# Performance work log

Hardware: AMD Instinct MI355X
Metric: run time of the kernel (lower is better)

Reference implementation:

```python
import jax, jax.numpy as jnp
import numpy as np

NEG = -1000000000.0
TEMP = 0.5
K = 15
EPS = 1e-5


def _bn(x, g, b):
    # BatchNorm1d in training mode: batch mean, biased variance
    mu = jnp.mean(x, axis=0)
    var = jnp.mean((x - mu) ** 2, axis=0)
    return (x - mu) * jax.lax.rsqrt(var + EPS) * g + b


def _lrelu(x):
    return jnp.where(x > 0, x, 0.2 * x)


def setup_inputs() -> dict:
    key = jax.random.key(0)
    ks = jax.random.split(key, 8)
    B, L = 131072, 50
    inp = {
        "z": jax.random.normal(ks[0], (B, L), jnp.float32),
        "u": jax.random.uniform(ks[1], (K, B, 25), jnp.float32),
        "W1": jax.random.normal(ks[2], (L, 128), jnp.float32) * 0.1,
        "b1": jnp.zeros((128,), jnp.float32),
        "g1": jnp.ones((128,), jnp.float32),
        "be1": jnp.zeros((128,), jnp.float32),
        "W2": jax.random.normal(ks[3], (128, 256), jnp.float32) * 0.1,
        "b2": jnp.zeros((256,), jnp.float32),
        "g2": jnp.ones((256,), jnp.float32),
        "be2": jnp.zeros((256,), jnp.float32),
        "W3": jax.random.normal(ks[4], (256, 128), jnp.float32) * 0.1,
        "b3": jnp.zeros((128,), jnp.float32),
        "g3": jnp.ones((128,), jnp.float32),
        "be3": jnp.zeros((128,), jnp.float32),
        "W4": jax.random.normal(ks[5], (128, 25), jnp.float32) * 0.1,
        "b4": jnp.zeros((25,), jnp.float32),
    }
    return inp


def reference(z, u, W1, b1, g1, be1, W2, b2, g2, be2, W3, b3, g3, be3, W4, b4):
    h = _lrelu(_bn(z @ W1 + b1, g1, be1))
    h = _lrelu(_bn(h @ W2 + b2, g2, be2))
    h = _lrelu(_bn(h @ W3 + b3, g3, be3))
    logits = h @ W4 + b4  # [B, 25]

    def step(mask, u_i):
        masked = jnp.where(mask, logits, NEG)
        noise = -jnp.log(-jnp.log(u_i))
        gumbel = (masked + noise) / TEMP
        probs = jax.nn.softmax(gumbel, axis=-1)
        idx = jnp.argmax(probs, axis=-1)  # [B]
        onehot = jax.nn.one_hot(idx, 25, dtype=bool)
        return mask & ~onehot, idx

    mask0 = jnp.ones(logits.shape, dtype=bool)
    _, idxs = jax.lax.scan(step, mask0, u)  # idxs: [K, B]
    selected = idxs.T.astype(jnp.float32) + 1.0  # [B, K], selected_idx + 1
    return (selected - 1.0) / 24.0
```

## Files before the change

kernel.cpp:

```cpp
#include <hip/hip_runtime.h>
#include <math.h>

#define BATCH 131072

template<int MT, int NT, int NSTORE, int TM, int TN, int BLK, bool AFFINE, bool STATS>
__global__ __launch_bounds__(BLK, 2)
void gemm_bn(const float* __restrict__ Ain, int K,
             const float* __restrict__ W, const float* __restrict__ bias,
             const float* __restrict__ sc, const float* __restrict__ sh,
             float* __restrict__ Xout,
             double* __restrict__ gsum, double* __restrict__ gsq)
{
    constexpr int KS  = 32;
    constexpr int MP  = MT + 4;
    constexpr int NP  = NT + 4;
    constexpr int NCG = NT / TN;
    constexpr int RG  = MT / TM;
    constexpr int NH  = TN / 4;
    static_assert(BLK == NCG * RG, "thread mapping");
    static_assert(!STATS || 2 * RG * NP <= KS * NP, "stats reuse of Bs");

    __shared__ float As[KS][MP];
    __shared__ float Bs[KS][NP];

    const int tid = threadIdx.x;
    const int r0  = blockIdx.x * MT;
    const int tx  = tid % NCG;
    const int ty  = tid / NCG;

    float acc[TM][TN] = {};

    const int KC = (K + KS - 1) / KS;
    for (int kc = 0; kc < KC; ++kc) {
        const int kbase = kc * KS;
        __syncthreads();
        constexpr int AL = MT * KS / BLK;
        #pragma unroll
        for (int l = 0; l < AL; ++l) {
            int idx = tid + l * BLK;
            int i = idx >> 5;
            int j = idx & 31;
            int gk = kbase + j;
            float v;
            if (AFFINE) {
                v = Ain[(size_t)(r0 + i) * K + gk];
                v = v * sc[gk] + sh[gk];
                v = v > 0.f ? v : 0.2f * v;
            } else {
                v = (gk < K) ? Ain[(size_t)(r0 + i) * K + gk] : 0.f;
            }
            As[j][i] = v;
        }
        constexpr int BL = NT * KS / BLK;
        #pragma unroll
        for (int l = 0; l < BL; ++l) {
            int idx = tid + l * BLK;
            int kk = idx / NT;
            int n  = idx % NT;
            int gk = kbase + kk;
            float v = 0.f;
            if (gk < K && n < NSTORE) v = W[(size_t)gk * NSTORE + n];
            Bs[kk][n] = v;
        }
        __syncthreads();
        #pragma unroll 2
        for (int k = 0; k < KS; ++k) {
            float a[TM], b[TN];
            #pragma unroll
            for (int i4 = 0; i4 < TM; i4 += 4)
                *reinterpret_cast<float4*>(&a[i4]) =
                    *reinterpret_cast<const float4*>(&As[k][ty * TM + i4]);
            #pragma unroll
            for (int h = 0; h < NH; ++h)
                *reinterpret_cast<float4*>(&b[h * 4]) =
                    *reinterpret_cast<const float4*>(&Bs[k][h * (NCG * 4) + tx * 4]);
            #pragma unroll
            for (int i = 0; i < TM; ++i)
                #pragma unroll
                for (int j = 0; j < TN; ++j)
                    acc[i][j] = fmaf(a[i], b[j], acc[i][j]);
        }
    }

    float bc[TN];
    #pragma unroll
    for (int j = 0; j < TN; ++j) {
        int gc = (j >> 2) * (NCG * 4) + tx * 4 + (j & 3);
        bc[j] = (gc < NSTORE) ? bias[gc] : 0.f;
    }
    float psum[TN] = {};
    float psq[TN]  = {};
    #pragma unroll
    for (int i = 0; i < TM; ++i) {
        int row = r0 + ty * TM + i;
        float x[TN];
        #pragma unroll
        for (int j = 0; j < TN; ++j) {
            x[j] = acc[i][j] + bc[j];
            psum[j] += x[j];
            psq[j]  += x[j] * x[j];
        }
        if (NSTORE == NT) {
            #pragma unroll
            for (int h = 0; h < NH; ++h) {
                float4 v = make_float4(x[h*4], x[h*4+1], x[h*4+2], x[h*4+3]);
                *reinterpret_cast<float4*>(
                    &Xout[(size_t)row * NSTORE + h * (NCG * 4) + tx * 4]) = v;
            }
        } else {
            #pragma unroll
            for (int j = 0; j < TN; ++j) {
                int gc = (j >> 2) * (NCG * 4) + tx * 4 + (j & 3);
                if (gc < NSTORE) Xout[(size_t)row * NSTORE + gc] = x[j];
            }
        }
    }

    if (STATS) {
        __syncthreads();
        float* S1 = &Bs[0][0];
        float* S2 = S1 + RG * NP;
        #pragma unroll
        for (int j = 0; j < TN; ++j) {
            int gc = (j >> 2) * (NCG * 4) + tx * 4 + (j & 3);
            S1[ty * NP + gc] = psum[j];
            S2[ty * NP + gc] = psq[j];
        }
        __syncthreads();
        if (tid < NT) {
            double s = 0.0, q = 0.0;
            #pragma unroll 4
            for (int t = 0; t < RG; ++t) {
                s += (double)S1[t * NP + tid];
                q += (double)S2[t * NP + tid];
            }
            atomicAdd(&gsum[tid], s);
            atomicAdd(&gsq[tid], q);
        }
    }
}

__global__ void finalize_bn(const double* __restrict__ sum, const double* __restrict__ sq,
                            const float* __restrict__ g, const float* __restrict__ be,
                            float* __restrict__ sc, float* __restrict__ sh, int N)
{
    int i = threadIdx.x;
    if (i < N) {
        const double inv = 1.0 / (double)BATCH;
        double mu  = sum[i] * inv;
        double var = sq[i] * inv - mu * mu;
        double s   = (double)g[i] / sqrt(var + 1e-5);
        sc[i] = (float)s;
        sh[i] = (float)((double)be[i] - mu * s);
    }
}

__global__ __launch_bounds__(256)
void gumbel_topk(const float* __restrict__ logits, const float* __restrict__ u,
                 float* __restrict__ out)
{
    __shared__ float lg[256 * 25];
    __shared__ float us[256 * 25];
    const int tid = threadIdx.x;
    const int r0  = blockIdx.x * 256;

    for (int idx = tid; idx < 256 * 25; idx += 256)
        lg[idx] = logits[(size_t)r0 * 25 + idx];
    __syncthreads();

    float myl[25];
    #pragma unroll
    for (int j = 0; j < 25; ++j) myl[j] = lg[tid * 25 + j];

    unsigned mask = 0x1FFFFFFu;
    for (int it = 0; it < 15; ++it) {
        __syncthreads();
        const float* uk = u + ((size_t)it * BATCH + r0) * 25;
        for (int idx = tid; idx < 256 * 25; idx += 256)
            us[idx] = uk[idx];
        __syncthreads();

        float best = -INFINITY;
        int bj = 0;
        #pragma unroll
        for (int j = 0; j < 25; ++j) {
            float uu = us[tid * 25 + j];
            float nz = -logf(-logf(uu));
            float v  = myl[j] + nz;
            v = ((mask >> j) & 1u) ? v : -INFINITY;
            if (v > best) { best = v; bj = j; }
        }
        mask &= ~(1u << bj);
        out[(size_t)(r0 + tid) * 15 + it] = (float)bj / 24.0f;
    }
}

extern "C" void kernel_launch(void* const* d_in, const int* in_sizes, int n_in,
                              void* d_out, int out_size, void* d_ws, size_t ws_size,
                              hipStream_t stream)
{
    (void)in_sizes; (void)n_in; (void)out_size; (void)ws_size;
    const float* z   = (const float*)d_in[0];
    const float* u   = (const float*)d_in[1];
    const float* W1  = (const float*)d_in[2];
    const float* b1  = (const float*)d_in[3];
    const float* g1  = (const float*)d_in[4];
    const float* be1 = (const float*)d_in[5];
    const float* W2  = (const float*)d_in[6];
    const float* b2  = (const float*)d_in[7];
    const float* g2  = (const float*)d_in[8];
    const float* be2 = (const float*)d_in[9];
    const float* W3  = (const float*)d_in[10];
    const float* b3  = (const float*)d_in[11];
    const float* g3  = (const float*)d_in[12];
    const float* be3 = (const float*)d_in[13];
    const float* W4  = (const float*)d_in[14];
    const float* b4  = (const float*)d_in[15];
    float* out = (float*)d_out;

    char* ws = (char*)d_ws;
    float* X2     = (float*)ws;
    float* XA     = (float*)(ws + (size_t)134217728);
    char*  statb  = ws + (size_t)134217728 + (size_t)67108864;
    double* sum1 = (double*)statb;      double* sq1 = sum1 + 128;
    double* sum2 = sq1 + 128;           double* sq2 = sum2 + 256;
    double* sum3 = sq2 + 256;           double* sq3 = sum3 + 128;
    float* sc1 = (float*)(sq3 + 128);   float* sh1 = sc1 + 128;
    float* sc2 = sh1 + 128;             float* sh2 = sc2 + 256;
    float* sc3 = sh2 + 256;             float* sh3 = sc3 + 128;
    float* logits = X2;

    hipMemsetAsync(statb, 0, 1024 * sizeof(double), stream);

    gemm_bn<256,128,128, 16,8, 256, false, true>
        <<<BATCH/256, 256, 0, stream>>>(z, 50, W1, b1, nullptr, nullptr, XA, sum1, sq1);
    finalize_bn<<<1, 256, 0, stream>>>(sum1, sq1, g1, be1, sc1, sh1, 128);

    gemm_bn<128,256,256, 16,8, 256, true, true>
        <<<BATCH/128, 256, 0, stream>>>(XA, 128, W2, b2, sc1, sh1, X2, sum2, sq2);
    finalize_bn<<<1, 256, 0, stream>>>(sum2, sq2, g2, be2, sc2, sh2, 256);

    gemm_bn<256,128,128, 16,8, 256, true, true>
        <<<BATCH/256, 256, 0, stream>>>(X2, 256, W3, b3, sc2, sh2, XA, sum3, sq3);
    finalize_bn<<<1, 256, 0, stream>>>(sum3, sq3, g3, be3, sc3, sh3, 128);

    gemm_bn<256,32,25, 8,4, 256, true, false>
        <<<BATCH/256, 256, 0, stream>>>(XA, 128, W4, b4, sc3, sh3, logits, nullptr, nullptr);

    gumbel_topk<<<BATCH/256, 256, 0, stream>>>(logits, u, out);
}
```

Measured before the change: 871.1 us.

## Fold BN finalize into GEMMs, vectorize tile loads, swizzle LDS, double-buffer gumbel noise

The separate finalize_bn launches are removed and each GEMM now computes the previous layer's BN scale and shift into shared memory. The A tile becomes row-major with float4 global loads and an XOR swizzle, the B tile also uses float4 loads, and the inner loop is restructured around 4-wide k chunks. K becomes a compile-time constant and the last layer's thread tiling changes. The gumbel kernel loads with float4 and double-buffers the uniform noise through registers so the next iteration's load overlaps the current compute. Risks include higher register pressure and redundant finalize work in every block.

```diff
diff --git a/kernel.cpp b/kernel.cpp
--- a/kernel.cpp
+++ b/kernel.cpp
@@ -3,82 +3,142 @@
 
 #define BATCH 131072
 
-template<int MT, int NT, int NSTORE, int TM, int TN, int BLK, bool AFFINE, bool STATS>
-__global__ __launch_bounds__(BLK, 2)
-void gemm_bn(const float* __restrict__ Ain, int K,
-             const float* __restrict__ W, const float* __restrict__ bias,
-             const float* __restrict__ sc, const float* __restrict__ sh,
-             float* __restrict__ Xout,
-             double* __restrict__ gsum, double* __restrict__ gsq)
+template<int MT, int NT, int NSTORE, int TM, int TN, int BLK, int KS, int K,
+         bool AFFINE, bool STATS>
+__global__ __launch_bounds__(BLK)
+void gemm_bn2(const float* __restrict__ Ain, const float* __restrict__ W,
+              const float* __restrict__ bias,
+              const float* __restrict__ gamma, const float* __restrict__ beta,
+              const double* __restrict__ prevSum, const double* __restrict__ prevSq,
+              float* __restrict__ Xout_g,
+              double* __restrict__ outSum, double* __restrict__ outSq)
 {
-    constexpr int KS  = 32;
-    constexpr int MP  = MT + 4;
-    constexpr int NP  = NT + 4;
-    constexpr int NCG = NT / TN;
-    constexpr int RG  = MT / TM;
-    constexpr int NH  = TN / 4;
-    static_assert(BLK == NCG * RG, "thread mapping");
-    static_assert(!STATS || 2 * RG * NP <= KS * NP, "stats reuse of Bs");
-
-    __shared__ float As[KS][MP];
-    __shared__ float Bs[KS][NP];
+    constexpr int KC   = (K + KS - 1) / KS;
+    constexpr bool TAIL = (K % KS) != 0;
+    constexpr int CPR  = KS / 4;
+    constexpr int NCG  = NT / TN;
+    constexpr int RG   = MT / TM;
+    constexpr int NH   = TN / 4;
+    constexpr int AL4  = MT * KS / 4 / BLK;
+    constexpr bool BVEC = (NT == NSTORE);
+    constexpr int BL4  = BVEC ? (KS * NT / 4 / BLK) : 1;
+    constexpr int BLS  = BVEC ? 1 : (KS * NT / BLK);
+    constexpr int HF   = (TM >= 8) ? 8 : TM;
+    static_assert(NCG * RG == BLK, "thread mapping");
+    static_assert(TM % HF == 0, "half split");
+    static_assert(!STATS || 2 * RG * NT <= KS * NT, "stats scratch fits Bs");
+
+    __shared__ float As[MT][KS];
+    __shared__ float Bs[KS][NT];
+    __shared__ float scs[AFFINE ? K : 1];
+    __shared__ float shs[AFFINE ? K : 1];
 
     const int tid = threadIdx.x;
     const int r0  = blockIdx.x * MT;
     const int tx  = tid % NCG;
     const int ty  = tid / NCG;
+    const int key = ty & 3;
+
+    if constexpr (AFFINE) {
+        for (int i = tid; i < K; i += BLK) {
+            const double inv = 1.0 / (double)BATCH;
+            double mu  = prevSum[i] * inv;
+            double var = prevSq[i] * inv - mu * mu;
+            double s   = (double)gamma[i] / sqrt(var + 1e-5);
+            scs[i] = (float)s;
+            shs[i] = (float)((double)beta[i] - mu * s);
+        }
+    }
 
     float acc[TM][TN] = {};
 
-    const int KC = (K + KS - 1) / KS;
     for (int kc = 0; kc < KC; ++kc) {
-        const int kbase = kc * KS;
-        __syncthreads();
-        constexpr int AL = MT * KS / BLK;
-        #pragma unroll
-        for (int l = 0; l < AL; ++l) {
+        const int kb = kc * KS;
+        __syncthreads();
+        #pragma unroll
+        for (int l = 0; l < AL4; ++l) {
             int idx = tid + l * BLK;
-            int i = idx >> 5;
-            int j = idx & 31;
-            int gk = kbase + j;
-            float v;
-            if (AFFINE) {
-                v = Ain[(size_t)(r0 + i) * K + gk];
-                v = v * sc[gk] + sh[gk];
-                v = v > 0.f ? v : 0.2f * v;
+            int row = idx / CPR;
+            int c4  = idx % CPR;
+            int gk  = kb + c4 * 4;
+            const float* gp = Ain + (size_t)(r0 + row) * K + gk;
+            float4 v;
+            if constexpr (!TAIL) {
+                v = *reinterpret_cast<const float4*>(gp);
             } else {
-                v = (gk < K) ? Ain[(size_t)(r0 + i) * K + gk] : 0.f;
-            }
-            As[j][i] = v;
-        }
-        constexpr int BL = NT * KS / BLK;
-        #pragma unroll
-        for (int l = 0; l < BL; ++l) {
-            int idx = tid + l * BLK;
-            int kk = idx / NT;
-            int n  = idx % NT;
-            int gk = kbase + kk;
-            float v = 0.f;
-            if (gk < K && n < NSTORE) v = W[(size_t)gk * NSTORE + n];
-            Bs[kk][n] = v;
-        }
-        __syncthreads();
-        #pragma unroll 2
-        for (int k = 0; k < KS; ++k) {
-            float a[TM], b[TN];
-            #pragma unroll
-            for (int i4 = 0; i4 < TM; i4 += 4)
-                *reinterpret_cast<float4*>(&a[i4]) =
-                    *reinterpret_cast<const float4*>(&As[k][ty * TM + i4]);
-            #pragma unroll
-            for (int h = 0; h < NH; ++h)
-                *reinterpret_cast<float4*>(&b[h * 4]) =
-                    *reinterpret_cast<const float4*>(&Bs[k][h * (NCG * 4) + tx * 4]);
-            #pragma unroll
-            for (int i = 0; i < TM; ++i)
+                if (gk + 4 <= K) v = *reinterpret_cast<const float4*>(gp);
+                else {
+                    float tt[4];
+                    #pragma unroll
+                    for (int c = 0; c < 4; ++c) tt[c] = (gk + c < K) ? gp[c] : 0.f;
+                    v = make_float4(tt[0], tt[1], tt[2], tt[3]);
+                }
+            }
+            if constexpr (AFFINE) {
+                float* vp = &v.x;
                 #pragma unroll
-                for (int j = 0; j < TN; ++j)
-                    acc[i][j] = fmaf(a[i], b[j], acc[i][j]);
+                for (int c = 0; c < 4; ++c) {
+                    float x = vp[c] * scs[gk + c] + shs[gk + c];
+                    vp[c] = x > 0.f ? x : 0.2f * x;
+                }
+            }
+            *reinterpret_cast<float4*>(&As[row][(c4 ^ ((row / TM) & 3)) * 4]) = v;
+        }
+        if constexpr (BVEC) {
+            #pragma unroll
+            for (int l = 0; l < BL4; ++l) {
+                int idx = tid + l * BLK;
+                int kk  = idx / (NT / 4);
+                int n4  = idx % (NT / 4);
+                int gk  = kb + kk;
+                float4 v;
+                if constexpr (!TAIL)
+                    v = *reinterpret_cast<const float4*>(W + (size_t)gk * NSTORE + n4 * 4);
+                else
+                    v = (gk < K)
+                      ? *reinterpret_cast<const float4*>(W + (size_t)gk * NSTORE + n4 * 4)
+                      : make_float4(0.f, 0.f, 0.f, 0.f);
+                *reinterpret_cast<float4*>(&Bs[kk][n4 * 4]) = v;
+            }
+        } else {
+            #pragma unroll
+            for (int l = 0; l < BLS; ++l) {
+                int idx = tid + l * BLK;
+                int kk  = idx / NT;
+                int n   = idx % NT;
+                int gk  = kb + kk;
+                Bs[kk][n] = (gk < K && n < NSTORE) ? W[(size_t)gk * NSTORE + n] : 0.f;
+            }
+        }
+        __syncthreads();
+        #pragma unroll
+        for (int k4 = 0; k4 < CPR; ++k4) {
+            const int pf = (k4 ^ key) * 4;
+            float4 bq[4][NH];
+            #pragma unroll
+            for (int kk = 0; kk < 4; ++kk)
+                #pragma unroll
+                for (int h = 0; h < NH; ++h)
+                    bq[kk][h] = *reinterpret_cast<const float4*>(
+                        &Bs[k4 * 4 + kk][h * (NCG * 4) + tx * 4]);
+            #pragma unroll
+            for (int hf = 0; hf < TM / HF; ++hf) {
+                float4 a4[HF];
+                #pragma unroll
+                for (int i = 0; i < HF; ++i)
+                    a4[i] = *reinterpret_cast<const float4*>(
+                        &As[ty * TM + hf * HF + i][pf]);
+                #pragma unroll
+                for (int kk = 0; kk < 4; ++kk)
+                    #pragma unroll
+                    for (int i = 0; i < HF; ++i) {
+                        const float av = (&a4[i].x)[kk];
+                        const float* bp = &bq[kk][0].x;
+                        #pragma unroll
+                        for (int j = 0; j < TN; ++j)
+                            acc[hf * HF + i][j] = fmaf(av, bp[j], acc[hf * HF + i][j]);
+                    }
+            }
         }
     }
 
@@ -88,8 +148,7 @@
         int gc = (j >> 2) * (NCG * 4) + tx * 4 + (j & 3);
         bc[j] = (gc < NSTORE) ? bias[gc] : 0.f;
     }
-    float psum[TN] = {};
-    float psq[TN]  = {};
+    float psum[TN] = {}, psq[TN] = {};
     #pragma unroll
     for (int i = 0; i < TM; ++i) {
         int row = r0 + ty * TM + i;
@@ -97,61 +156,44 @@
         #pragma unroll
         for (int j = 0; j < TN; ++j) {
             x[j] = acc[i][j] + bc[j];
-            psum[j] += x[j];
-            psq[j]  += x[j] * x[j];
-        }
-        if (NSTORE == NT) {
+            if (STATS) { psum[j] += x[j]; psq[j] += x[j] * x[j]; }
+        }
+        if constexpr (BVEC) {
             #pragma unroll
             for (int h = 0; h < NH; ++h) {
                 float4 v = make_float4(x[h*4], x[h*4+1], x[h*4+2], x[h*4+3]);
                 *reinterpret_cast<float4*>(
-                    &Xout[(size_t)row * NSTORE + h * (NCG * 4) + tx * 4]) = v;
+                    &Xout_g[(size_t)row * NSTORE + h * (NCG * 4) + tx * 4]) = v;
             }
         } else {
             #pragma unroll
             for (int j = 0; j < TN; ++j) {
                 int gc = (j >> 2) * (NCG * 4) + tx * 4 + (j & 3);
-                if (gc < NSTORE) Xout[(size_t)row * NSTORE + gc] = x[j];
-            }
-        }
-    }
-
-    if (STATS) {
+                if (gc < NSTORE) Xout_g[(size_t)row * NSTORE + gc] = x[j];
+            }
+        }
+    }
+    if constexpr (STATS) {
         __syncthreads();
         float* S1 = &Bs[0][0];
-        float* S2 = S1 + RG * NP;
+        float* S2 = S1 + RG * NT;
         #pragma unroll
         for (int j = 0; j < TN; ++j) {
             int gc = (j >> 2) * (NCG * 4) + tx * 4 + (j & 3);
-            S1[ty * NP + gc] = psum[j];
-            S2[ty * NP + gc] = psq[j];
+            S1[ty * NT + gc] = psum[j];
+            S2[ty * NT + gc] = psq[j];
         }
         __syncthreads();
         if (tid < NT) {
             double s = 0.0, q = 0.0;
             #pragma unroll 4
             for (int t = 0; t < RG; ++t) {
-                s += (double)S1[t * NP + tid];
-                q += (double)S2[t * NP + tid];
-            }
-            atomicAdd(&gsum[tid], s);
-            atomicAdd(&gsq[tid], q);
-        }
-    }
-}
-
-__global__ void finalize_bn(const double* __restrict__ sum, const double* __restrict__ sq,
-                            const float* __restrict__ g, const float* __restrict__ be,
-                            float* __restrict__ sc, float* __restrict__ sh, int N)
-{
-    int i = threadIdx.x;
-    if (i < N) {
-        const double inv = 1.0 / (double)BATCH;
-        double mu  = sum[i] * inv;
-        double var = sq[i] * inv - mu * mu;
-        double s   = (double)g[i] / sqrt(var + 1e-5);
-        sc[i] = (float)s;
-        sh[i] = (float)((double)be[i] - mu * s);
+                s += (double)S1[t * NT + tid];
+                q += (double)S2[t * NT + tid];
+            }
+            atomicAdd(&outSum[tid], s);
+            atomicAdd(&outSq[tid], q);
+        }
     }
 }
 
@@ -159,13 +201,27 @@
 void gumbel_topk(const float* __restrict__ logits, const float* __restrict__ u,
                  float* __restrict__ out)
 {
-    __shared__ float lg[256 * 25];
-    __shared__ float us[256 * 25];
+    __shared__ __align__(16) float lg[256 * 25];
+    __shared__ __align__(16) float us[2][256 * 25];
     const int tid = threadIdx.x;
     const int r0  = blockIdx.x * 256;
 
-    for (int idx = tid; idx < 256 * 25; idx += 256)
-        lg[idx] = logits[(size_t)r0 * 25 + idx];
+    {
+        const float4* src = reinterpret_cast<const float4*>(logits + (size_t)r0 * 25);
+        float4* dst = reinterpret_cast<float4*>(lg);
+        #pragma unroll
+        for (int l = 0; l < 7; ++l) {
+            int i = tid + l * 256;
+            if (i < 1600) dst[i] = src[i];
+        }
+        const float4* u0 = reinterpret_cast<const float4*>(u + (size_t)r0 * 25);
+        float4* d0 = reinterpret_cast<float4*>(us[0]);
+        #pragma unroll
+        for (int l = 0; l < 7; ++l) {
+            int i = tid + l * 256;
+            if (i < 1600) d0[i] = u0[i];
+        }
+    }
     __syncthreads();
 
     float myl[25];
@@ -174,17 +230,24 @@
 
     unsigned mask = 0x1FFFFFFu;
     for (int it = 0; it < 15; ++it) {
-        __syncthreads();
-        const float* uk = u + ((size_t)it * BATCH + r0) * 25;
-        for (int idx = tid; idx < 256 * 25; idx += 256)
-            us[idx] = uk[idx];
-        __syncthreads();
+        const int cur = it & 1;
+        float4 t[7];
+        const bool have = (it + 1) < 15;
+        if (have) {
+            const float4* un = reinterpret_cast<const float4*>(
+                u + ((size_t)(it + 1) * BATCH + r0) * 25);
+            #pragma unroll
+            for (int l = 0; l < 7; ++l) {
+                int i = tid + l * 256;
+                if (i < 1600) t[l] = un[i];
+            }
+        }
 
         float best = -INFINITY;
         int bj = 0;
         #pragma unroll
         for (int j = 0; j < 25; ++j) {
-            float uu = us[tid * 25 + j];
+            float uu = us[cur][tid * 25 + j];
             float nz = -logf(-logf(uu));
             float v  = myl[j] + nz;
             v = ((mask >> j) & 1u) ? v : -INFINITY;
@@ -192,6 +255,16 @@
         }
         mask &= ~(1u << bj);
         out[(size_t)(r0 + tid) * 15 + it] = (float)bj / 24.0f;
+
+        if (have) {
+            float4* dn = reinterpret_cast<float4*>(us[cur ^ 1]);
+            #pragma unroll
+            for (int l = 0; l < 7; ++l) {
+                int i = tid + l * 256;
+                if (i < 1600) dn[i] = t[l];
+            }
+        }
+        __syncthreads();
     }
 }
 
@@ -225,27 +298,25 @@
     double* sum1 = (double*)statb;      double* sq1 = sum1 + 128;
     double* sum2 = sq1 + 128;           double* sq2 = sum2 + 256;
     double* sum3 = sq2 + 256;           double* sq3 = sum3 + 128;
-    float* sc1 = (float*)(sq3 + 128);   float* sh1 = sc1 + 128;
-    float* sc2 = sh1 + 128;             float* sh2 = sc2 + 256;
-    float* sc3 = sh2 + 256;             float* sh3 = sc3 + 128;
     float* logits = X2;
 
-    hipMemsetAsync(statb, 0, 1024 * sizeof(double), stream);
-
-    gemm_bn<256,128,128, 16,8, 256, false, true>
-        <<<BATCH/256, 256, 0, stream>>>(z, 50, W1, b1, nullptr, nullptr, XA, sum1, sq1);
-    finalize_bn<<<1, 256, 0, stream>>>(sum1, sq1, g1, be1, sc1, sh1, 128);
-
-    gemm_bn<128,256,256, 16,8, 256, true, true>
-        <<<BATCH/128, 256, 0, stream>>>(XA, 128, W2, b2, sc1, sh1, X2, sum2, sq2);
-    finalize_bn<<<1, 256, 0, stream>>>(sum2, sq2, g2, be2, sc2, sh2, 256);
-
-    gemm_bn<256,128,128, 16,8, 256, true, true>
-        <<<BATCH/256, 256, 0, stream>>>(X2, 256, W3, b3, sc2, sh2, XA, sum3, sq3);
-    finalize_bn<<<1, 256, 0, stream>>>(sum3, sq3, g3, be3, sc3, sh3, 128);
-
-    gemm_bn<256,32,25, 8,4, 256, true, false>
-        <<<BATCH/256, 256, 0, stream>>>(XA, 128, W4, b4, sc3, sh3, logits, nullptr, nullptr);
+    (void)hipMemsetAsync(statb, 0, 1024 * sizeof(double), stream);
+
+    gemm_bn2<256,128,128, 16,8, 256, 32, 50, false, true>
+        <<<BATCH/256, 256, 0, stream>>>(z, W1, b1, nullptr, nullptr,
+                                        nullptr, nullptr, XA, sum1, sq1);
+
+    gemm_bn2<128,256,256, 16,8, 256, 32, 128, true, true>
+        <<<BATCH/128, 256, 0, stream>>>(XA, W2, b2, g1, be1,
+                                        sum1, sq1, X2, sum2, sq2);
+
+    gemm_bn2<256,128,128, 16,8, 256, 32, 256, true, true>
+        <<<BATCH/256, 256, 0, stream>>>(X2, W3, b3, g2, be2,
+                                        sum2, sq2, XA, sum3, sq3);
+
+    gemm_bn2<256,32,25, 4,8, 256, 32, 128, true, false>
+        <<<BATCH/256, 256, 0, stream>>>(XA, W4, b4, g3, be3,
+                                        sum3, sq3, logits, nullptr, nullptr);
 
     gumbel_topk<<<BATCH/256, 256, 0, stream>>>(logits, u, out);
 }
```

Measured after the change: 738.6 us. -15.2%, faster.
